# Optimization experiments

Hardware: AMD Instinct MI355X
Metric: run time of the kernel (lower is better)

Reference implementation:

```python
import jax, jax.numpy as jnp
import numpy as np

B, S, E, H = 2, 2048, 1024, 16
D = E // H
NORM = np.float32(np.sqrt(E))


def setup_inputs() -> dict:
    key = jax.random.key(0)
    ks = jax.random.split(key, 5)
    scale = np.float32(E ** -0.5)
    x = jax.random.normal(ks[0], (B, S, E), jnp.float32)
    Wq = jax.random.normal(ks[1], (E, E), jnp.float32) * scale
    Wk = jax.random.normal(ks[2], (E, E), jnp.float32) * scale
    Wv = jax.random.normal(ks[3], (E, E), jnp.float32) * scale
    Wo = jax.random.normal(ks[4], (E, E), jnp.float32) * scale
    return {"encoded_vectors": x, "Wq": Wq, "Wk": Wk, "Wv": Wv, "Wo": Wo}


def reference(encoded_vectors, Wq, Wk, Wv, Wo):
    x = encoded_vectors                      # [B,S,E]
    q = x @ Wq.T                             # nn.Linear(bias=False): x @ W^T
    k = x @ Wk.T
    v = x @ Wv.T
    skip_val = v                             # residual is the v-projection output
    qh = q.reshape(B, S, H, D).transpose(0, 2, 1, 3)  # [B,H,S,D]
    kh = k.reshape(B, S, H, D).transpose(0, 2, 1, 3)
    vh = v.reshape(B, S, H, D).transpose(0, 2, 1, 3)
    scores = jnp.einsum('bhsd,bhtd->bhst', qh, kh)    # [B,H,S,S]
    # causal additive mask: -inf strictly above the diagonal (triu, k=1)
    mask = jnp.triu(jnp.full((S, S), -jnp.inf, jnp.float32), 1)
    logits = (scores + mask) / NORM          # mask added BEFORE scaling, per source
    p = jax.nn.softmax(logits, axis=-1)
    # faithful to torch.einsum('stuu,stuv->stuv'): diagonal of p scales v elementwise
    attn = jnp.einsum('bhss,bhsd->bhsd', p, vh)       # [B,H,S,D]
    out = attn.transpose(0, 2, 1, 3).reshape(B, S, E)
    return out @ Wo.T + skip_val
```

## Files before the change

kernel.cpp:

```cpp
#include <hip/hip_runtime.h>
#include <hip/hip_bf16.h>

#define B_ 2
#define S_ 2048
#define E_ 1024
#define H_ 16
#define D_ 64
#define M_ (B_*S_)

typedef unsigned short u16;
typedef __attribute__((ext_vector_type(8))) short short8;
typedef __attribute__((ext_vector_type(4))) short short4v;
typedef __attribute__((ext_vector_type(4))) float f32x4;

__device__ __forceinline__ float b2f(u16 u) {
    union { float f; unsigned int i; } x; x.i = ((unsigned int)u) << 16; return x.f;
}
__device__ __forceinline__ u16 f2b(float f) {
    union { float f; unsigned int i; } x; x.f = f;
    unsigned int r = x.i + 0x7fffu + ((x.i >> 16) & 1u);
    return (u16)(r >> 16);
}
__device__ __forceinline__ int imin(int a, int b) { return a < b ? a : b; }

#if __has_builtin(__builtin_amdgcn_exp2f)
__device__ __forceinline__ float ex2(float x) { return __builtin_amdgcn_exp2f(x); }
#else
__device__ __forceinline__ float ex2(float x) {
    float r; asm("v_exp_f32 %0, %1" : "=v"(r) : "v"(x)); return r;
}
#endif

__global__ __launch_bounds__(256)
void cvt_kernel(const float* __restrict__ X,
                const float* __restrict__ Wq, const float* __restrict__ Wk,
                const float* __restrict__ Wv, const float* __restrict__ Wo,
                u16* __restrict__ Xb, u16* __restrict__ Wqb, u16* __restrict__ Wkb,
                u16* __restrict__ Wvb, u16* __restrict__ Wob)
{
    int bid = blockIdx.x;
    const float* src; u16* dst; int blk;
    if (bid < 4096) { src = X; dst = Xb; blk = bid; }
    else {
        int w = (bid - 4096) >> 10;
        blk = (bid - 4096) & 1023;
        src = (w == 0) ? Wq : (w == 1) ? Wk : (w == 2) ? Wv : Wo;
        dst = (w == 0) ? Wqb : (w == 1) ? Wkb : (w == 2) ? Wvb : Wob;
    }
    size_t i4 = (size_t)blk * 256 + threadIdx.x;
    float4 v = ((const float4*)src)[i4];
    short4v o;
    o.x = (short)f2b(v.x); o.y = (short)f2b(v.y);
    o.z = (short)f2b(v.z); o.w = (short)f2b(v.w);
    *(short4v*)(dst + i4 * 4) = o;
}

#define BN 128
#define BK 32

template<int CH>
__device__ __forceinline__ void stage2(const u16* __restrict__ gbase, u16* lds,
                                       int ldg, int wave, int lane)
{
    #pragma unroll
    for (int n = 0; n < CH; ++n) {
        int chunk = wave * CH + n;
        int r = chunk * 16 + (lane >> 2);
        int slot = lane & 3;
        int c = slot ^ ((r >> 1) & 3);
        const u16* g = gbase + (size_t)r * ldg + c * 8;
        u16* l = lds + chunk * 512;
        __builtin_amdgcn_global_load_lds(
            (const __attribute__((address_space(1))) unsigned int*)g,
            (__attribute__((address_space(3))) unsigned int*)l, 16, 0, 0);
    }
}

template<bool F32OUT, int BMT>
__device__ __forceinline__ void gemm_bt_core(
    const u16* __restrict__ A, const u16* __restrict__ Bm,
    void* __restrict__ Cv, const u16* __restrict__ skip,
    int N, int Kd, int bm, int bn)
{
    constexpr int NI = BMT / 32;
    __shared__ u16 lA[BMT * BK];
    __shared__ u16 lB[BN * BK];
    const int tid  = threadIdx.x;
    const int wave = tid >> 6, lane = tid & 63;
    const int quad = lane >> 4, l16 = lane & 15;
    const int wm = (wave & 1) * (BMT / 2), wn = (wave >> 1) * 64;

    f32x4 acc[NI][4];
    #pragma unroll
    for (int i = 0; i < NI; ++i)
        #pragma unroll
        for (int j = 0; j < 4; ++j)
            acc[i][j] = (f32x4){0.f, 0.f, 0.f, 0.f};

    for (int k0 = 0; k0 < Kd; k0 += BK) {
        stage2<BMT / 64>(A  + (size_t)bm * Kd + k0, lA, Kd, wave, lane);
        stage2<2>(Bm + (size_t)bn * Kd + k0, lB, Kd, wave, lane);
        __syncthreads();
        short8 af[NI], bf[4];
        #pragma unroll
        for (int i = 0; i < NI; ++i) {
            int R = wm + i * 16 + l16;
            af[i] = *(const short8*)&lA[R * 32 + ((quad ^ ((R >> 1) & 3)) * 8)];
        }
        #pragma unroll
        for (int j = 0; j < 4; ++j) {
            int R = wn + j * 16 + l16;
            bf[j] = *(const short8*)&lB[R * 32 + ((quad ^ ((R >> 1) & 3)) * 8)];
        }
        #pragma unroll
        for (int i = 0; i < NI; ++i)
            #pragma unroll
            for (int j = 0; j < 4; ++j)
                acc[i][j] = __builtin_amdgcn_mfma_f32_16x16x32_bf16(af[i], bf[j], acc[i][j], 0, 0, 0);
        __syncthreads();
    }

    #pragma unroll
    for (int i = 0; i < NI; ++i) {
        #pragma unroll
        for (int j = 0; j < 4; ++j) {
            int row0 = bm + wm + i * 16 + quad * 4;
            int col  = bn + wn + j * 16 + l16;
            #pragma unroll
            for (int r = 0; r < 4; ++r) {
                size_t idx = (size_t)(row0 + r) * N + col;
                float v = acc[i][j][r];
                if (skip) v += b2f(skip[idx]);
                if (F32OUT) ((float*)Cv)[idx] = v;
                else        ((u16*)Cv)[idx]   = f2b(v);
            }
        }
    }
}

__global__ __launch_bounds__(256, 3)
void qkv_kernel(const u16* __restrict__ X,
                const u16* __restrict__ Wq, const u16* __restrict__ Wk, const u16* __restrict__ Wv,
                u16* __restrict__ Q, u16* __restrict__ K, u16* __restrict__ V)
{
    const u16* W = (blockIdx.z == 0) ? Wq : (blockIdx.z == 1) ? Wk : Wv;
    u16* C = (blockIdx.z == 0) ? Q : (blockIdx.z == 1) ? K : V;
    gemm_bt_core<false, 128>(X, W, C, nullptr, E_, E_, blockIdx.x * 128, blockIdx.y * BN);
}

__global__ __launch_bounds__(256, 4)
void out_kernel(const u16* __restrict__ An, const u16* __restrict__ Wo,
                const u16* __restrict__ V, float* __restrict__ Out)
{
    gemm_bt_core<true, 64>(An, Wo, Out, V, E_, E_, blockIdx.x * 64, blockIdx.y * BN);
}

__global__ __launch_bounds__(512, 4)
void attn_diag_kernel(const u16* __restrict__ Q, const u16* __restrict__ Kp,
                      const u16* __restrict__ V, u16* __restrict__ An)
{
    __shared__ float lred[8][8][16];
    __shared__ float dv[8][16];
    __shared__ float pv[8][16];
    const int bid = blockIdx.x;
    const int xcd = bid & 7;
    const int i   = bid >> 3;
    const int g   = i & 15;
    const int bh  = ((i >> 4) << 3) + xcd;
    const int b = bh >> 4, h = bh & 15;
    const int wave = threadIdx.x >> 6, lane = threadIdx.x & 63;
    const int quad = lane >> 4, l16 = lane & 15;
    const float CE = 0.04508422002778f;

    short8 aq0[8], aq1[8];
    #pragma unroll
    for (int j = 0; j < 8; ++j) {
        const u16* qp = Q + ((size_t)(b * S_) + (g + 16 * j) * 16 + l16) * E_ + h * D_ + quad * 8;
        aq0[j] = *(const short8*)qp;
        aq1[j] = *(const short8*)(qp + 32);
    }

    float l[8][4];
    #pragma unroll
    for (int j = 0; j < 8; ++j)
        #pragma unroll
        for (int r = 0; r < 4; ++r) l[j][r] = 0.f;

    const int TMAX = g + 112;
    const u16* kcol = Kp + ((size_t)(b * S_) + l16) * E_ + h * D_ + quad * 8;

    short8 K0c, K1c;
    {
        const u16* ka = kcol + (size_t)(wave * 16) * E_;
        K0c = *(const short8*)ka; K1c = *(const short8*)(ka + 32);
    }
    for (int ti = wave; ti <= TMAX; ti += 8) {
        f32x4 sc[8];
        #pragma unroll
        for (int j = 0; j < 8; ++j) {
            if (g + 16 * j >= ti) {
                f32x4 t = (f32x4){0.f,0.f,0.f,0.f};
                t = __builtin_amdgcn_mfma_f32_16x16x32_bf16(aq0[j], K0c, t, 0, 0, 0);
                t = __builtin_amdgcn_mfma_f32_16x16x32_bf16(aq1[j], K1c, t, 0, 0, 0);
                sc[j] = t;
            }
        }
        {
            const u16* ka = kcol + (size_t)(imin(ti + 8, TMAX) * 16) * E_;
            K0c = *(const short8*)ka; K1c = *(const short8*)(ka + 32);
        }
        #pragma unroll
        for (int j = 0; j < 8; ++j) {
            int st = g + 16 * j;
            if (st > ti) {
                #pragma unroll
                for (int r = 0; r < 4; ++r) l[j][r] += ex2(sc[j][r] * CE);
            } else if (st == ti) {
                #pragma unroll
                for (int r = 0; r < 4; ++r) {
                    int sg = quad * 4 + r;
                    float e = (l16 <= sg) ? ex2(sc[j][r] * CE) : 0.f;
                    l[j][r] += e;
                    if (l16 == sg) dv[j][sg] = e;
                }
            }
        }
    }

    #pragma unroll
    for (int j = 0; j < 8; ++j)
        #pragma unroll
        for (int r = 0; r < 4; ++r) {
            float v = l[j][r];
            v += __shfl_xor(v, 1); v += __shfl_xor(v, 2);
            v += __shfl_xor(v, 4); v += __shfl_xor(v, 8);
            if (l16 == 0) lred[wave][j][quad * 4 + r] = v;
        }
    __syncthreads();
    if (threadIdx.x < 128) {
        int j = threadIdx.x >> 4, row = threadIdx.x & 15;
        float lsum = 0.f;
        #pragma unroll
        for (int w = 0; w < 8; ++w) lsum += lred[w][j][row];
        pv[j][row] = dv[j][row] / lsum;
    }
    __syncthreads();

    #pragma unroll
    for (int k = 0; k < 2; ++k) {
        int c = threadIdx.x + k * 512;
        int row = c >> 3, col8 = (c & 7) * 8;
        int j = row >> 4, r = row & 15;
        int s = (g + 16 * j) * 16 + r;
        size_t idx = ((size_t)(b * S_) + s) * E_ + h * D_ + col8;
        float p = pv[j][r];
        int4 pk = *(const int4*)(V + idx);
        u16* u = (u16*)&pk;
        #pragma unroll
        for (int q = 0; q < 8; ++q) u[q] = f2b(b2f(u[q]) * p);
        *(int4*)(An + idx) = pk;
    }
}

extern "C" void kernel_launch(void* const* d_in, const int* in_sizes, int n_in,
                              void* d_out, int out_size, void* d_ws, size_t ws_size,
                              hipStream_t stream)
{
    const float* X  = (const float*)d_in[0];
    const float* Wq = (const float*)d_in[1];
    const float* Wk = (const float*)d_in[2];
    const float* Wv = (const float*)d_in[3];
    const float* Wo = (const float*)d_in[4];
    float* Out = (float*)d_out;

    u16* Xb  = (u16*)d_ws;
    u16* Wqb = Xb  + (size_t)M_ * E_;
    u16* Wkb = Wqb + (size_t)E_ * E_;
    u16* Wvb = Wkb + (size_t)E_ * E_;
    u16* Wob = Wvb + (size_t)E_ * E_;
    u16* Q   = Wob + (size_t)E_ * E_;
    u16* K   = Q   + (size_t)M_ * E_;
    u16* V   = K   + (size_t)M_ * E_;
    u16* An  = V   + (size_t)M_ * E_;

    cvt_kernel<<<dim3(4096 + 4 * 1024), dim3(256), 0, stream>>>(X, Wq, Wk, Wv, Wo,
                                                                Xb, Wqb, Wkb, Wvb, Wob);
    qkv_kernel<<<dim3(M_/128, E_/BN, 3), dim3(256), 0, stream>>>(Xb, Wqb, Wkb, Wvb, Q, K, V);
    attn_diag_kernel<<<dim3(512), dim3(512), 0, stream>>>(Q, K, V, An);
    out_kernel<<<dim3(M_/64, E_/BN), dim3(256), 0, stream>>>(An, Wob, V, Out);
}
```

Before: 183.8 us.

## Split causal attention into triangular 128x128 tiles with atomic row-sum reduction

```diff
diff --git a/kernel.cpp b/kernel.cpp
--- a/kernel.cpp
+++ b/kernel.cpp
@@ -21,7 +21,6 @@
     unsigned int r = x.i + 0x7fffu + ((x.i >> 16) & 1u);
     return (u16)(r >> 16);
 }
-__device__ __forceinline__ int imin(int a, int b) { return a < b ? a : b; }
 
 #if __has_builtin(__builtin_amdgcn_exp2f)
 __device__ __forceinline__ float ex2(float x) { return __builtin_amdgcn_exp2f(x); }
@@ -36,9 +35,15 @@
                 const float* __restrict__ Wq, const float* __restrict__ Wk,
                 const float* __restrict__ Wv, const float* __restrict__ Wo,
                 u16* __restrict__ Xb, u16* __restrict__ Wqb, u16* __restrict__ Wkb,
-                u16* __restrict__ Wvb, u16* __restrict__ Wob)
+                u16* __restrict__ Wvb, u16* __restrict__ Wob,
+                float* __restrict__ lsum)
 {
     int bid = blockIdx.x;
+    if (bid >= 8192) {
+        size_t i4 = (size_t)(bid - 8192) * 256 + threadIdx.x;
+        ((float4*)lsum)[i4] = make_float4(0.f, 0.f, 0.f, 0.f);
+        return;
+    }
     const float* src; u16* dst; int blk;
     if (bid < 4096) { src = X; dst = Xb; blk = bid; }
     else {
@@ -76,11 +81,10 @@
     }
 }
 
-template<bool F32OUT, int BMT>
-__device__ __forceinline__ void gemm_bt_core(
+template<int BMT>
+__device__ __forceinline__ void gemm_bt_acc(
     const u16* __restrict__ A, const u16* __restrict__ Bm,
-    void* __restrict__ Cv, const u16* __restrict__ skip,
-    int N, int Kd, int bm, int bn)
+    int Kd, int bm, int bn, f32x4 (*acc)[4])
 {
     constexpr int NI = BMT / 32;
     __shared__ u16 lA[BMT * BK];
@@ -90,13 +94,6 @@
     const int quad = lane >> 4, l16 = lane & 15;
     const int wm = (wave & 1) * (BMT / 2), wn = (wave >> 1) * 64;
 
-    f32x4 acc[NI][4];
-    #pragma unroll
-    for (int i = 0; i < NI; ++i)
-        #pragma unroll
-        for (int j = 0; j < 4; ++j)
-            acc[i][j] = (f32x4){0.f, 0.f, 0.f, 0.f};
-
     for (int k0 = 0; k0 < Kd; k0 += BK) {
         stage2<BMT / 64>(A  + (size_t)bm * Kd + k0, lA, Kd, wave, lane);
         stage2<2>(Bm + (size_t)bn * Kd + k0, lB, Kd, wave, lane);
@@ -119,147 +116,181 @@
                 acc[i][j] = __builtin_amdgcn_mfma_f32_16x16x32_bf16(af[i], bf[j], acc[i][j], 0, 0, 0);
         __syncthreads();
     }
-
-    #pragma unroll
-    for (int i = 0; i < NI; ++i) {
+}
+
+__global__ __launch_bounds__(256, 3)
+void qkv_kernel(const u16* __restrict__ X,
+                const u16* __restrict__ Wq, const u16* __restrict__ Wk, const u16* __restrict__ Wv,
+                u16* __restrict__ Q, u16* __restrict__ K, u16* __restrict__ V)
+{
+    const u16* W = (blockIdx.z == 0) ? Wq : (blockIdx.z == 1) ? Wk : Wv;
+    u16* C = (blockIdx.z == 0) ? Q : (blockIdx.z == 1) ? K : V;
+    const int bm = blockIdx.x * 128, bn = blockIdx.y * BN;
+    f32x4 acc[4][4];
+    #pragma unroll
+    for (int i = 0; i < 4; ++i)
+        #pragma unroll
+        for (int j = 0; j < 4; ++j) acc[i][j] = (f32x4){0.f,0.f,0.f,0.f};
+    gemm_bt_acc<128>(X, W, E_, bm, bn, acc);
+
+    const int wave = threadIdx.x >> 6, lane = threadIdx.x & 63;
+    const int quad = lane >> 4, l16 = lane & 15;
+    const int wm = (wave & 1) * 64, wn = (wave >> 1) * 64;
+    #pragma unroll
+    for (int i = 0; i < 4; ++i)
+        #pragma unroll
+        for (int j = 0; j < 4; ++j) {
+            int row0 = bm + wm + i * 16 + quad * 4;
+            int col  = bn + wn + j * 16 + l16;
+            #pragma unroll
+            for (int r = 0; r < 4; ++r)
+                C[(size_t)(row0 + r) * E_ + col] = f2b(acc[i][j][r]);
+        }
+}
+
+__global__ __launch_bounds__(256, 4)
+void out_kernel(const u16* __restrict__ An, const u16* __restrict__ Wo,
+                const u16* __restrict__ V, float* __restrict__ Out)
+{
+    const int bm = blockIdx.x * 64, bn = blockIdx.y * BN;
+    f32x4 acc[2][4];
+    #pragma unroll
+    for (int i = 0; i < 2; ++i)
+        #pragma unroll
+        for (int j = 0; j < 4; ++j) acc[i][j] = (f32x4){0.f,0.f,0.f,0.f};
+    gemm_bt_acc<64>(An, Wo, E_, bm, bn, acc);
+
+    const int wave = threadIdx.x >> 6, lane = threadIdx.x & 63;
+    const int quad = lane >> 4, l16 = lane & 15;
+    const int wm = (wave & 1) * 32, wn = (wave >> 1) * 64;
+    #pragma unroll
+    for (int i = 0; i < 2; ++i)
         #pragma unroll
         for (int j = 0; j < 4; ++j) {
             int row0 = bm + wm + i * 16 + quad * 4;
             int col  = bn + wn + j * 16 + l16;
             #pragma unroll
             for (int r = 0; r < 4; ++r) {
-                size_t idx = (size_t)(row0 + r) * N + col;
-                float v = acc[i][j][r];
-                if (skip) v += b2f(skip[idx]);
-                if (F32OUT) ((float*)Cv)[idx] = v;
-                else        ((u16*)Cv)[idx]   = f2b(v);
+                size_t idx = (size_t)(row0 + r) * E_ + col;
+                Out[idx] = acc[i][j][r] + b2f(V[idx]);
             }
         }
-    }
-}
-
-__global__ __launch_bounds__(256, 3)
-void qkv_kernel(const u16* __restrict__ X,
-                const u16* __restrict__ Wq, const u16* __restrict__ Wk, const u16* __restrict__ Wv,
-                u16* __restrict__ Q, u16* __restrict__ K, u16* __restrict__ V)
-{
-    const u16* W = (blockIdx.z == 0) ? Wq : (blockIdx.z == 1) ? Wk : Wv;
-    u16* C = (blockIdx.z == 0) ? Q : (blockIdx.z == 1) ? K : V;
-    gemm_bt_core<false, 128>(X, W, C, nullptr, E_, E_, blockIdx.x * 128, blockIdx.y * BN);
 }
 
 __global__ __launch_bounds__(256, 4)
-void out_kernel(const u16* __restrict__ An, const u16* __restrict__ Wo,
-                const u16* __restrict__ V, float* __restrict__ Out)
-{
-    gemm_bt_core<true, 64>(An, Wo, Out, V, E_, E_, blockIdx.x * 64, blockIdx.y * BN);
-}
-
-__global__ __launch_bounds__(512, 4)
-void attn_diag_kernel(const u16* __restrict__ Q, const u16* __restrict__ Kp,
-                      const u16* __restrict__ V, u16* __restrict__ An)
-{
-    __shared__ float lred[8][8][16];
-    __shared__ float dv[8][16];
-    __shared__ float pv[8][16];
-    const int bid = blockIdx.x;
-    const int xcd = bid & 7;
-    const int i   = bid >> 3;
-    const int g   = i & 15;
-    const int bh  = ((i >> 4) << 3) + xcd;
+void attn_tiles_kernel(const u16* __restrict__ Q, const u16* __restrict__ Kp,
+                       float* __restrict__ lsum, float* __restrict__ ed)
+{
+    __shared__ u16 lK[128 * 64];
+    const int tau = blockIdx.x;
+    const int bh  = blockIdx.y;
     const int b = bh >> 4, h = bh & 15;
+    int ii = 0;
+    while ((ii + 1) * (ii + 2) / 2 <= tau) ++ii;
+    const int jj = tau - ii * (ii + 1) / 2;
+    const bool diag = (ii == jj);
     const int wave = threadIdx.x >> 6, lane = threadIdx.x & 63;
     const int quad = lane >> 4, l16 = lane & 15;
     const float CE = 0.04508422002778f;
 
-    short8 aq0[8], aq1[8];
-    #pragma unroll
-    for (int j = 0; j < 8; ++j) {
-        const u16* qp = Q + ((size_t)(b * S_) + (g + 16 * j) * 16 + l16) * E_ + h * D_ + quad * 8;
-        aq0[j] = *(const short8*)qp;
-        aq1[j] = *(const short8*)(qp + 32);
-    }
-
-    float l[8][4];
-    #pragma unroll
-    for (int j = 0; j < 8; ++j)
-        #pragma unroll
-        for (int r = 0; r < 4; ++r) l[j][r] = 0.f;
-
-    const int TMAX = g + 112;
-    const u16* kcol = Kp + ((size_t)(b * S_) + l16) * E_ + h * D_ + quad * 8;
-
-    short8 K0c, K1c;
-    {
-        const u16* ka = kcol + (size_t)(wave * 16) * E_;
-        K0c = *(const short8*)ka; K1c = *(const short8*)(ka + 32);
-    }
-    for (int ti = wave; ti <= TMAX; ti += 8) {
-        f32x4 sc[8];
-        #pragma unroll
-        for (int j = 0; j < 8; ++j) {
-            if (g + 16 * j >= ti) {
-                f32x4 t = (f32x4){0.f,0.f,0.f,0.f};
-                t = __builtin_amdgcn_mfma_f32_16x16x32_bf16(aq0[j], K0c, t, 0, 0, 0);
-                t = __builtin_amdgcn_mfma_f32_16x16x32_bf16(aq1[j], K1c, t, 0, 0, 0);
-                sc[j] = t;
+    const u16* kg = Kp + ((size_t)(b * S_) + jj * 128) * E_ + h * D_;
+    #pragma unroll
+    for (int m4 = 0; m4 < 4; ++m4) {
+        int q = m4 * 256 + wave * 64 + lane;
+        int slot = q & 3, hr = q >> 2;
+        int f = hr >> 7, r = hr & 127;
+        int c = f * 4 + (slot ^ ((r >> 1) & 3));
+        const u16* g = kg + (size_t)r * E_ + c * 8;
+        u16* l = lK + (size_t)(m4 * 256 + wave * 64) * 8;
+        __builtin_amdgcn_global_load_lds(
+            (const __attribute__((address_space(1))) unsigned int*)g,
+            (__attribute__((address_space(3))) unsigned int*)l, 16, 0, 0);
+    }
+
+    short8 aq[2][2];
+    #pragma unroll
+    for (int m = 0; m < 2; ++m) {
+        const u16* qp = Q + ((size_t)(b * S_) + ii * 128 + wave * 32 + m * 16 + l16) * E_
+                        + h * D_ + quad * 8;
+        aq[m][0] = *(const short8*)qp;
+        aq[m][1] = *(const short8*)(qp + 32);
+    }
+    __syncthreads();
+
+    f32x4 acc[2][8];
+    #pragma unroll
+    for (int m = 0; m < 2; ++m)
+        #pragma unroll
+        for (int n = 0; n < 8; ++n) acc[m][n] = (f32x4){0.f,0.f,0.f,0.f};
+
+    #pragma unroll
+    for (int nt = 0; nt < 8; ++nt) {
+        int R = nt * 16 + l16;
+        int sw = (R >> 1) & 3;
+        short8 bk0 = *(const short8*)&lK[((0 * 128 + R) * 4 + (quad ^ sw)) * 8];
+        short8 bk1 = *(const short8*)&lK[((1 * 128 + R) * 4 + (quad ^ sw)) * 8];
+        #pragma unroll
+        for (int m = 0; m < 2; ++m) {
+            acc[m][nt] = __builtin_amdgcn_mfma_f32_16x16x32_bf16(aq[m][0], bk0, acc[m][nt], 0, 0, 0);
+            acc[m][nt] = __builtin_amdgcn_mfma_f32_16x16x32_bf16(aq[m][1], bk1, acc[m][nt], 0, 0, 0);
+        }
+    }
+
+    float rs[2][4];
+    #pragma unroll
+    for (int m = 0; m < 2; ++m)
+        #pragma unroll
+        for (int r = 0; r < 4; ++r) rs[m][r] = 0.f;
+
+    #pragma unroll
+    for (int m = 0; m < 2; ++m)
+        #pragma unroll
+        for (int nt = 0; nt < 8; ++nt)
+            #pragma unroll
+            for (int r = 0; r < 4; ++r) {
+                float e = ex2(acc[m][nt][r] * CE);
+                if (diag) {
+                    int srow = wave * 32 + m * 16 + quad * 4 + r;
+                    int tcol = nt * 16 + l16;
+                    if (tcol > srow) e = 0.f;
+                    if (tcol == srow)
+                        ed[(size_t)bh * S_ + ii * 128 + srow] = e;
+                }
+                rs[m][r] += e;
             }
-        }
-        {
-            const u16* ka = kcol + (size_t)(imin(ti + 8, TMAX) * 16) * E_;
-            K0c = *(const short8*)ka; K1c = *(const short8*)(ka + 32);
-        }
-        #pragma unroll
-        for (int j = 0; j < 8; ++j) {
-            int st = g + 16 * j;
-            if (st > ti) {
-                #pragma unroll
-                for (int r = 0; r < 4; ++r) l[j][r] += ex2(sc[j][r] * CE);
-            } else if (st == ti) {
-                #pragma unroll
-                for (int r = 0; r < 4; ++r) {
-                    int sg = quad * 4 + r;
-                    float e = (l16 <= sg) ? ex2(sc[j][r] * CE) : 0.f;
-                    l[j][r] += e;
-                    if (l16 == sg) dv[j][sg] = e;
-                }
-            }
-        }
-    }
-
-    #pragma unroll
-    for (int j = 0; j < 8; ++j)
+
+    #pragma unroll
+    for (int m = 0; m < 2; ++m)
         #pragma unroll
         for (int r = 0; r < 4; ++r) {
-            float v = l[j][r];
+            float v = rs[m][r];
             v += __shfl_xor(v, 1); v += __shfl_xor(v, 2);
             v += __shfl_xor(v, 4); v += __shfl_xor(v, 8);
-            if (l16 == 0) lred[wave][j][quad * 4 + r] = v;
-        }
-    __syncthreads();
-    if (threadIdx.x < 128) {
-        int j = threadIdx.x >> 4, row = threadIdx.x & 15;
-        float lsum = 0.f;
-        #pragma unroll
-        for (int w = 0; w < 8; ++w) lsum += lred[w][j][row];
-        pv[j][row] = dv[j][row] / lsum;
-    }
-    __syncthreads();
-
-    #pragma unroll
-    for (int k = 0; k < 2; ++k) {
-        int c = threadIdx.x + k * 512;
-        int row = c >> 3, col8 = (c & 7) * 8;
-        int j = row >> 4, r = row & 15;
-        int s = (g + 16 * j) * 16 + r;
-        size_t idx = ((size_t)(b * S_) + s) * E_ + h * D_ + col8;
-        float p = pv[j][r];
-        int4 pk = *(const int4*)(V + idx);
-        u16* u = (u16*)&pk;
-        #pragma unroll
-        for (int q = 0; q < 8; ++q) u[q] = f2b(b2f(u[q]) * p);
-        *(int4*)(An + idx) = pk;
-    }
+            if (l16 == 0) {
+                int srow = ii * 128 + wave * 32 + m * 16 + quad * 4 + r;
+                atomicAdd(&lsum[(size_t)bh * S_ + srow], v);
+            }
+        }
+}
+
+__global__ __launch_bounds__(256)
+void scale_v_kernel(const u16* __restrict__ V, const float* __restrict__ lsum,
+                    const float* __restrict__ ed, u16* __restrict__ An)
+{
+    size_t i = (size_t)blockIdx.x * blockDim.x + threadIdx.x;
+    size_t base = i * 8;
+    int e = (int)(base & (E_ - 1));
+    size_t bs = base >> 10;
+    int h = e >> 6;
+    int b = (int)(bs >> 11);
+    int s = (int)(bs & (S_ - 1));
+    size_t li = ((size_t)(b * H_ + h)) * S_ + s;
+    float p = ed[li] / lsum[li];
+    int4 pk = *(const int4*)(V + base);
+    u16* u = (u16*)&pk;
+    #pragma unroll
+    for (int j = 0; j < 8; ++j) u[j] = f2b(b2f(u[j]) * p);
+    *(int4*)(An + base) = pk;
 }
 
 extern "C" void kernel_launch(void* const* d_in, const int* in_sizes, int n_in,
@@ -282,10 +313,13 @@
     u16* K   = Q   + (size_t)M_ * E_;
     u16* V   = K   + (size_t)M_ * E_;
     u16* An  = V   + (size_t)M_ * E_;
-
-    cvt_kernel<<<dim3(4096 + 4 * 1024), dim3(256), 0, stream>>>(X, Wq, Wk, Wv, Wo,
-                                                                Xb, Wqb, Wkb, Wvb, Wob);
+    float* lsum = (float*)(An + (size_t)M_ * E_);
+    float* ed   = lsum + (size_t)B_ * H_ * S_;
+
+    cvt_kernel<<<dim3(8192 + 64), dim3(256), 0, stream>>>(X, Wq, Wk, Wv, Wo,
+                                                          Xb, Wqb, Wkb, Wvb, Wob, lsum);
     qkv_kernel<<<dim3(M_/128, E_/BN, 3), dim3(256), 0, stream>>>(Xb, Wqb, Wkb, Wvb, Q, K, V);
-    attn_diag_kernel<<<dim3(512), dim3(512), 0, stream>>>(Q, K, V, An);
+    attn_tiles_kernel<<<dim3(136, B_*H_), dim3(256), 0, stream>>>(Q, K, lsum, ed);
+    scale_v_kernel<<<dim3((M_*E_/8)/256), dim3(256), 0, stream>>>(V, lsum, ed, An);
     out_kernel<<<dim3(M_/64, E_/BN), dim3(256), 0, stream>>>(An, Wob, V, Out);
 }
```

After: 161.1 us. -12.4%, faster.
